# Kernel tuning notes

Hardware: AMD Instinct MI355X
Metric: run time of the kernel (lower is better)

The kernel has to match this reference:

```python
import jax, jax.numpy as jnp
import numpy as np

NV = 20000; NC = 20000; E = 500000
IN_SHAPE = 2; PE_DIM = 8; HID = 64; NL = 3
EPS = 1e-7  # GENConv message eps


def _lin(x, w, b):
    return x @ w + b


def _encode(x, pe, ew, eb, pw1, pb1, pw2, pb2):
    # relu(cat([Linear(x), 0.5*(pe_mlp(pe)+pe_mlp(-pe))], dim=1))
    def pe_mlp(p):
        return _lin(jax.nn.relu(_lin(p, pw1, pb1)), pw2, pb2)
    h = jnp.concatenate([_lin(x, ew, eb), 0.5 * (pe_mlp(pe) + pe_mlp(-pe))], axis=1)
    return jax.nn.relu(h)


def _genconv(x_src, x_dst, src, dst, ewt, lew, leb, w1, b1, w2, b2, n_dst):
    # GENConv(aggr='softmax', t=1, norm=None, msg_norm=False, edge_dim=1)
    msg = jax.nn.relu(x_src[src] + _lin(ewt, lew, leb)) + EPS  # [E, HID]
    m = jax.ops.segment_max(msg, dst, num_segments=n_dst)      # stable segment softmax
    ex = jnp.exp(msg - m[dst])
    s = jax.ops.segment_sum(ex, dst, num_segments=n_dst)
    agg = jax.ops.segment_sum(ex / (s[dst] + 1e-16) * msg, dst, num_segments=n_dst)
    out = agg + x_dst
    return _lin(jax.nn.relu(_lin(out, w1, b1)), w2, b2)  # MLP [hid -> 2hid -> hid]


def setup_inputs() -> dict:
    key = jax.random.key(0)
    ks = iter(jax.random.split(key, 64))
    d = {}
    d['x_vals'] = jax.random.normal(next(ks), (NV, IN_SHAPE), jnp.float32)
    d['x_cons'] = jax.random.normal(next(ks), (NC, IN_SHAPE), jnp.float32)
    d['pe_vals'] = jax.random.normal(next(ks), (NV, PE_DIM), jnp.float32)
    d['pe_cons'] = jax.random.normal(next(ks), (NC, PE_DIM), jnp.float32)
    d['edge_index_v2c'] = jnp.stack([
        jax.random.randint(next(ks), (E,), 0, NV),
        jax.random.randint(next(ks), (E,), 0, NC)])
    d['edge_index_c2v'] = jnp.stack([
        jax.random.randint(next(ks), (E,), 0, NC),
        jax.random.randint(next(ks), (E,), 0, NV)])
    d['edge_weight_v2c'] = jax.random.normal(next(ks), (E, 1), jnp.float32)
    d['edge_weight_c2v'] = jax.random.normal(next(ks), (E, 1), jnp.float32)
    def p(shape):
        return jax.random.normal(next(ks), shape, jnp.float32) * 0.05
    for k_ in ['vals', 'cons']:
        d[f'enc_{k_}_w'] = p((IN_SHAPE, HID // 2)); d[f'enc_{k_}_b'] = p((HID // 2,))
        d[f'pe_{k_}_w1'] = p((PE_DIM, HID)); d[f'pe_{k_}_b1'] = p((HID,))
        d[f'pe_{k_}_w2'] = p((HID, HID // 2)); d[f'pe_{k_}_b2'] = p((HID // 2,))
    for c in ['v2c', 'c2v']:
        d[f'{c}_edge_w'] = p((NL, 1, HID)); d[f'{c}_edge_b'] = p((NL, HID))
        d[f'{c}_w1'] = p((NL, HID, 2 * HID)); d[f'{c}_b1'] = p((NL, 2 * HID))
        d[f'{c}_w2'] = p((NL, 2 * HID, HID)); d[f'{c}_b2'] = p((NL, HID))
    for k_ in ['vals', 'cons']:
        d[f'pred_{k_}_w1'] = p((HID, HID)); d[f'pred_{k_}_b1'] = p((HID,))
        d[f'pred_{k_}_w2'] = p((HID, 1)); d[f'pred_{k_}_b2'] = p((1,))
    return d


def reference(x_vals, x_cons, pe_vals, pe_cons, edge_index_v2c, edge_index_c2v,
              edge_weight_v2c, edge_weight_c2v,
              enc_vals_w, enc_vals_b, pe_vals_w1, pe_vals_b1, pe_vals_w2, pe_vals_b2,
              enc_cons_w, enc_cons_b, pe_cons_w1, pe_cons_b1, pe_cons_w2, pe_cons_b2,
              v2c_edge_w, v2c_edge_b, v2c_w1, v2c_b1, v2c_w2, v2c_b2,
              c2v_edge_w, c2v_edge_b, c2v_w1, c2v_b1, c2v_w2, c2v_b2,
              pred_vals_w1, pred_vals_b1, pred_vals_w2, pred_vals_b2,
              pred_cons_w1, pred_cons_b1, pred_cons_w2, pred_cons_b2):
    vals = _encode(x_vals, pe_vals, enc_vals_w, enc_vals_b,
                   pe_vals_w1, pe_vals_b1, pe_vals_w2, pe_vals_b2)
    cons = _encode(x_cons, pe_cons, enc_cons_w, enc_cons_b,
                   pe_cons_w1, pe_cons_b1, pe_cons_w2, pe_cons_b2)
    hv, hc = [], []
    for i in range(NL):
        cons = _genconv(vals, cons, edge_index_v2c[0], edge_index_v2c[1],
                        edge_weight_v2c, v2c_edge_w[i], v2c_edge_b[i],
                        v2c_w1[i], v2c_b1[i], v2c_w2[i], v2c_b2[i], NC)
        vals = _genconv(cons, vals, edge_index_c2v[0], edge_index_c2v[1],
                        edge_weight_c2v, c2v_edge_w[i], c2v_edge_b[i],
                        c2v_w1[i], c2v_b1[i], c2v_w2[i], c2v_b2[i], NV)
        hc.append(cons); hv.append(vals)
    V = jnp.stack(hv)  # [NL, NV, HID]
    C = jnp.stack(hc)  # [NL, NC, HID]
    pv = _lin(jax.nn.relu(_lin(V, pred_vals_w1, pred_vals_b1)), pred_vals_w2, pred_vals_b2)
    pc = _lin(jax.nn.relu(_lin(C, pred_cons_w1, pred_cons_b1)), pred_cons_w2, pred_cons_b2)
    return pv[..., 0].T, pc[..., 0].T  # [NV, NL], [NC, NL]
```

## Files before the change

### kernel.cpp

```cpp
#include <hip/hip_runtime.h>

#define NVN 20000
#define NCN 20000
#define NE  500000
#define HID 64
#define NLAYER 3
#define TN 40
#define BSH 8
#define NB 79
#define P1E 2048

__device__ __forceinline__ float relu_(float x) { return fmaxf(x, 0.0f); }

__global__ __launch_bounds__(256) void binhist_kernel(
    const int* __restrict__ dstA, const int* __restrict__ dstB,
    int* __restrict__ binszA, int* __restrict__ binszB)
{
    __shared__ int cA[NB], cB[NB];
    int t = threadIdx.x;
    int e0 = blockIdx.x * P1E;
    if (t < NB) { cA[t] = 0; cB[t] = 0; }
    __syncthreads();
    for (int i = t; i < P1E; i += 256) {
        int e = e0 + i;
        if (e < NE) {
            atomicAdd(&cA[dstA[e] >> BSH], 1);
            atomicAdd(&cB[dstB[e] >> BSH], 1);
        }
    }
    __syncthreads();
    if (t < NB) {
        if (cA[t] > 0) atomicAdd(&binszA[t], cA[t]);
        if (cB[t] > 0) atomicAdd(&binszB[t], cB[t]);
    }
}

__global__ __launch_bounds__(256) void binscan_kernel(
    const int* __restrict__ binszA, int* __restrict__ binbaseA, int* __restrict__ bincurA,
    const int* __restrict__ binszB, int* __restrict__ binbaseB, int* __restrict__ bincurB)
{
    const int* binsz = blockIdx.x ? binszB : binszA;
    int* binbase     = blockIdx.x ? binbaseB : binbaseA;
    int* bincur      = blockIdx.x ? bincurB : bincurA;
    __shared__ int p[256];
    int t = threadIdx.x;
    p[t] = (t < NB) ? binsz[t] : 0;
    __syncthreads();
    for (int off = 1; off < 256; off <<= 1) {
        int v = (t >= off) ? p[t - off] : 0;
        __syncthreads();
        p[t] += v;
        __syncthreads();
    }
    if (t < NB) { int b = (t == 0) ? 0 : p[t - 1]; binbase[t] = b; bincur[t] = b; }
    if (t == NB) binbase[NB] = p[NB - 1];
}

__global__ __launch_bounds__(256) void scatter_p1_kernel(
    const int* __restrict__ eiA, const float* __restrict__ ewA,
    int* __restrict__ bincurA, int2* __restrict__ stageA,
    const int* __restrict__ eiB, const float* __restrict__ ewB,
    int* __restrict__ bincurB, int2* __restrict__ stageB)
{
    __shared__ int rnk[P1E];
    __shared__ int cnt[NB], base_[NB];
    int t = threadIdx.x;
    int e0 = blockIdx.x * P1E;

    for (int g = 0; g < 2; ++g) {
        const int* ei   = g ? eiB : eiA;
        const float* ew = g ? ewB : ewA;
        int* bincur     = g ? bincurB : bincurA;
        int2* stage     = g ? stageB : stageA;

        if (t < NB) cnt[t] = 0;
        __syncthreads();
        for (int i = t; i < P1E; i += 256) {
            int e = e0 + i;
            if (e < NE) {
                int d = ei[NE + e];
                rnk[i] = atomicAdd(&cnt[d >> BSH], 1);
            }
        }
        __syncthreads();
        if (t < NB && cnt[t] > 0) base_[t] = atomicAdd(&bincur[t], cnt[t]);
        __syncthreads();
        for (int i = t; i < P1E; i += 256) {
            int e = e0 + i;
            if (e < NE) {
                int s = ei[e], d = ei[NE + e];
                float w = ew[e];
                stage[base_[d >> BSH] + rnk[i]] =
                    make_int2((int)((unsigned)s | ((unsigned)d << 16)), __float_as_int(w));
            }
        }
        __syncthreads();
    }
}

__global__ __launch_bounds__(1024) void scatter_p2_kernel(
    const int* __restrict__ binbaseA, const int2* __restrict__ stageA,
    int* __restrict__ rowptrA, int2* __restrict__ pairA,
    const int* __restrict__ binbaseB, const int2* __restrict__ stageB,
    int* __restrict__ rowptrB, int2* __restrict__ pairB)
{
    __shared__ int deg[256], pfx[256], cur[256];
    int g = blockIdx.x / NB;
    int b = blockIdx.x % NB;
    const int* binbase = g ? binbaseB : binbaseA;
    const int2* stage  = g ? stageB : stageA;
    int* rowptr        = g ? rowptrB : rowptrA;
    int2* pair         = g ? pairB : pairA;

    int d0 = b << BSH;
    int d1 = min(d0 + 256, NCN);
    int nd = d1 - d0;
    int t = threadIdx.x;
    int estart = binbase[b], eend = binbase[b + 1];

    if (t < 256) deg[t] = 0;
    __syncthreads();
    for (int e = estart + t; e < eend; e += 1024) {
        int dst = (int)((unsigned)stage[e].x >> 16);
        atomicAdd(&deg[dst - d0], 1);
    }
    __syncthreads();
    if (t < 256) pfx[t] = deg[t];
    __syncthreads();
    for (int off = 1; off < 256; off <<= 1) {
        int v = (t >= off && t < 256) ? pfx[t - off] : 0;
        __syncthreads();
        if (t < 256) pfx[t] += v;
        __syncthreads();
    }
    if (t < nd) {
        int ex = estart + pfx[t] - deg[t];
        rowptr[d0 + t] = ex;
        cur[t] = ex;
    }
    if (t == 0) rowptr[d1] = eend;
    __syncthreads();
    for (int e = estart + t; e < eend; e += 1024) {
        int2 s = stage[e];
        unsigned u = (unsigned)s.x;
        int src = (int)(u & 0xFFFFu);
        int dst = (int)(u >> 16);
        int p = atomicAdd(&cur[dst - d0], 1);
        pair[p] = make_int2(src, s.y);
    }
}

__global__ __launch_bounds__(256) void encode2_kernel(
    const float* __restrict__ xv, const float* __restrict__ pev,
    const float* __restrict__ ewv, const float* __restrict__ ebv,
    const float* __restrict__ pw1v, const float* __restrict__ pb1v,
    const float* __restrict__ pw2v, const float* __restrict__ pb2v,
    const float* __restrict__ xc, const float* __restrict__ pec,
    const float* __restrict__ ewc, const float* __restrict__ ebc,
    const float* __restrict__ pw1c, const float* __restrict__ pb1c,
    const float* __restrict__ pw2c, const float* __restrict__ pb2c,
    float* __restrict__ outv, float* __restrict__ outc)
{
    __shared__ float sh[4][64];
    const int VB = (NVN + 3) / 4;
    int wave = threadIdx.x >> 6, lane = threadIdx.x & 63;
    int b = blockIdx.x;
    bool isC = (b >= VB);
    const float* x   = isC ? xc : xv;
    const float* pe  = isC ? pec : pev;
    const float* ew  = isC ? ewc : ewv;
    const float* eb  = isC ? ebc : ebv;
    const float* pw1 = isC ? pw1c : pw1v;
    const float* pb1 = isC ? pb1c : pb1v;
    const float* pw2 = isC ? pw2c : pw2v;
    const float* pb2 = isC ? pb2c : pb2v;
    float* out = isC ? outc : outv;
    int N = isC ? NCN : NVN;
    int n = (isC ? b - VB : b) * 4 + wave;
    if (n >= N) return;

    float accp = pb1[lane], accm = accp;
#pragma unroll
    for (int k = 0; k < 8; ++k) {
        float p = pe[n * 8 + k];
        float w = pw1[k * 64 + lane];
        accp += p * w;
        accm -= p * w;
    }
    float hs = 0.5f * (relu_(accp) + relu_(accm));
    float* my = sh[wave];
    my[lane] = hs;
    __builtin_amdgcn_wave_barrier();

    int col = lane & 31;
    float peo = pb2[col];
#pragma unroll
    for (int k = 0; k < 64; k += 4) {
        float4 hv = *(const float4*)(my + k);
        peo = fmaf(hv.x, pw2[(k + 0) * 32 + col], peo);
        peo = fmaf(hv.y, pw2[(k + 1) * 32 + col], peo);
        peo = fmaf(hv.z, pw2[(k + 2) * 32 + col], peo);
        peo = fmaf(hv.w, pw2[(k + 3) * 32 + col], peo);
    }
    float lino = x[n * 2 + 0] * ew[col] + x[n * 2 + 1] * ew[32 + col] + eb[col];
    float h = (lane < 32) ? lino : peo;
    out[n * 64 + lane] = relu_(h);
}

__global__ __launch_bounds__(256) void edge_agg_kernel(
    const float* __restrict__ xsrc,
    const float* __restrict__ xdst,
    const int* __restrict__ rowptr,
    const int2* __restrict__ pair,
    const float* __restrict__ lew,
    const float* __restrict__ leb,
    float* __restrict__ oa,
    int N)
{
    int wave = threadIdx.x >> 6, lane = threadIdx.x & 63;
    int n = blockIdx.x * 4 + wave;
    if (n >= N) return;

    int start = rowptr[n], end = rowptr[n + 1];
    float lw = lew[lane], lb = leb[lane];
    float xd = xdst[n * 64 + lane];

    float m0 = -1e30f, den0 = 0.0f, num0 = 0.0f;
    float m1 = -1e30f, den1 = 0.0f, num1 = 0.0f;
    int j = start;
    for (; j + 16 <= end; j += 16) {
        int idx[16]; float wv[16], msg[16];
#pragma unroll
        for (int c = 0; c < 16; ++c) {
            int2 p = pair[j + c];
            idx[c] = p.x;
            wv[c] = __int_as_float(p.y);
        }
#pragma unroll
        for (int c = 0; c < 16; ++c) {
            float xv = xsrc[idx[c] * 64 + lane];
            msg[c] = relu_(fmaf(wv[c], lw, xv + lb)) + 1e-7f;
        }
        {
            float a0 = fmaxf(msg[0], msg[1]), a1 = fmaxf(msg[2], msg[3]);
            float a2 = fmaxf(msg[4], msg[5]), a3 = fmaxf(msg[6], msg[7]);
            float mnew = fmaxf(m0, fmaxf(fmaxf(a0, a1), fmaxf(a2, a3)));
            float sc = __expf(m0 - mnew);
            float cd = 0.0f, cn = 0.0f;
#pragma unroll
            for (int c = 0; c < 8; ++c) {
                float e = __expf(msg[c] - mnew);
                cd += e;
                cn = fmaf(e, msg[c], cn);
            }
            den0 = fmaf(den0, sc, cd);
            num0 = fmaf(num0, sc, cn);
            m0 = mnew;
        }
        {
            float a0 = fmaxf(msg[8], msg[9]), a1 = fmaxf(msg[10], msg[11]);
            float a2 = fmaxf(msg[12], msg[13]), a3 = fmaxf(msg[14], msg[15]);
            float mnew = fmaxf(m1, fmaxf(fmaxf(a0, a1), fmaxf(a2, a3)));
            float sc = __expf(m1 - mnew);
            float cd = 0.0f, cn = 0.0f;
#pragma unroll
            for (int c = 8; c < 16; ++c) {
                float e = __expf(msg[c] - mnew);
                cd += e;
                cn = fmaf(e, msg[c], cn);
            }
            den1 = fmaf(den1, sc, cd);
            num1 = fmaf(num1, sc, cn);
            m1 = mnew;
        }
    }
    for (; j + 8 <= end; j += 8) {
        int idx[8]; float wv[8], msg[8];
#pragma unroll
        for (int c = 0; c < 8; ++c) {
            int2 p = pair[j + c];
            idx[c] = p.x;
            wv[c] = __int_as_float(p.y);
        }
#pragma unroll
        for (int c = 0; c < 8; ++c) {
            float xv = xsrc[idx[c] * 64 + lane];
            msg[c] = relu_(fmaf(wv[c], lw, xv + lb)) + 1e-7f;
        }
        float a0 = fmaxf(msg[0], msg[1]), a1 = fmaxf(msg[2], msg[3]);
        float a2 = fmaxf(msg[4], msg[5]), a3 = fmaxf(msg[6], msg[7]);
        float mnew = fmaxf(m0, fmaxf(fmaxf(a0, a1), fmaxf(a2, a3)));
        float sc = __expf(m0 - mnew);
        float cd = 0.0f, cn = 0.0f;
#pragma unroll
        for (int c = 0; c < 8; ++c) {
            float e = __expf(msg[c] - mnew);
            cd += e;
            cn = fmaf(e, msg[c], cn);
        }
        den0 = fmaf(den0, sc, cd);
        num0 = fmaf(num0, sc, cn);
        m0 = mnew;
    }
    for (; j < end; ++j) {
        int2 p = pair[j];
        float xv = xsrc[p.x * 64 + lane];
        float msg = relu_(fmaf(__int_as_float(p.y), lw, xv + lb)) + 1e-7f;
        float mnew = fmaxf(m0, msg);
        float sc = __expf(m0 - mnew);
        float e = __expf(msg - mnew);
        den0 = fmaf(den0, sc, e);
        num0 = fmaf(num0, sc, e * msg);
        m0 = mnew;
    }
    float M = fmaxf(m0, m1);
    float s0 = __expf(m0 - M), s1 = __expf(m1 - M);
    float den = den0 * s0 + den1 * s1;
    float num = num0 * s0 + num1 * s1;

    oa[n * 64 + lane] = num / (den + 1e-16f) + xd;
}

__global__ __launch_bounds__(256) void mlp_kernel(
    const float* __restrict__ oa,
    float* __restrict__ feat,
    const float* __restrict__ w1,
    const float* __restrict__ b1,
    const float* __restrict__ w2,
    const float* __restrict__ b2,
    const float* __restrict__ pw1,
    const float* __restrict__ pb1,
    const float* __restrict__ pw2,
    const float* __restrict__ pb2,
    float* __restrict__ outp,
    int N, int layer)
{
    __shared__ float w1s[64 * 128];
    __shared__ float w2s[128 * 64];
    __shared__ float pw1s[64 * 64];
    __shared__ float b1s[128];
    __shared__ float b2s[64];
    __shared__ float pb1s[64];
    __shared__ float pw2s[64];
    __shared__ float act[TN][68];
    __shared__ float hid[TN][132];

    int tid = threadIdx.x;
    for (int i = tid; i < 64 * 128; i += 256) w1s[i] = w1[i];
    for (int i = tid; i < 128 * 64; i += 256) w2s[i] = w2[i];
    for (int i = tid; i < 64 * 64; i += 256) pw1s[i] = pw1[i];
    if (tid < 128) b1s[tid] = b1[tid];
    if (tid < 64) { b2s[tid] = b2[tid]; pb1s[tid] = pb1[tid]; pw2s[tid] = pw2[tid]; }
    float pb2v = pb2[0];

    int o4 = (tid & 31) * 4;
    int o2 = (tid & 31) * 2;
    int n5 = (tid >> 5) * 5;
    __syncthreads();

    int ntiles = N / TN;
    for (int tile = blockIdx.x; tile < ntiles; tile += gridDim.x) {
        int base = tile * TN;
        {
            const float* g = oa + (size_t)base * 64;
            for (int i = tid; i < TN * 64; i += 256)
                act[i >> 6][i & 63] = g[i];
        }
        __syncthreads();

        {
            float acc[5][4];
#pragma unroll
            for (int i = 0; i < 5; ++i)
#pragma unroll
                for (int q = 0; q < 4; ++q) acc[i][q] = b1s[o4 + q];
            for (int k = 0; k < 64; k += 4) {
                float4 a[5];
#pragma unroll
                for (int i = 0; i < 5; ++i) a[i] = *(const float4*)&act[n5 + i][k];
                float4 w0 = *(const float4*)&w1s[(k + 0) * 128 + o4];
                float4 wq1 = *(const float4*)&w1s[(k + 1) * 128 + o4];
                float4 wq2 = *(const float4*)&w1s[(k + 2) * 128 + o4];
                float4 wq3 = *(const float4*)&w1s[(k + 3) * 128 + o4];
#pragma unroll
                for (int i = 0; i < 5; ++i) {
                    acc[i][0] = fmaf(a[i].x, w0.x, acc[i][0]);
                    acc[i][1] = fmaf(a[i].x, w0.y, acc[i][1]);
                    acc[i][2] = fmaf(a[i].x, w0.z, acc[i][2]);
                    acc[i][3] = fmaf(a[i].x, w0.w, acc[i][3]);
                    acc[i][0] = fmaf(a[i].y, wq1.x, acc[i][0]);
                    acc[i][1] = fmaf(a[i].y, wq1.y, acc[i][1]);
                    acc[i][2] = fmaf(a[i].y, wq1.z, acc[i][2]);
                    acc[i][3] = fmaf(a[i].y, wq1.w, acc[i][3]);
                    acc[i][0] = fmaf(a[i].z, wq2.x, acc[i][0]);
                    acc[i][1] = fmaf(a[i].z, wq2.y, acc[i][1]);
                    acc[i][2] = fmaf(a[i].z, wq2.z, acc[i][2]);
                    acc[i][3] = fmaf(a[i].z, wq2.w, acc[i][3]);
                    acc[i][0] = fmaf(a[i].w, wq3.x, acc[i][0]);
                    acc[i][1] = fmaf(a[i].w, wq3.y, acc[i][1]);
                    acc[i][2] = fmaf(a[i].w, wq3.z, acc[i][2]);
                    acc[i][3] = fmaf(a[i].w, wq3.w, acc[i][3]);
                }
            }
#pragma unroll
            for (int i = 0; i < 5; ++i) {
                float4 h4 = make_float4(relu_(acc[i][0]), relu_(acc[i][1]),
                                        relu_(acc[i][2]), relu_(acc[i][3]));
                *(float4*)&hid[n5 + i][o4] = h4;
            }
        }
        __syncthreads();

        {
            float acc[5][2];
#pragma unroll
            for (int i = 0; i < 5; ++i) { acc[i][0] = b2s[o2]; acc[i][1] = b2s[o2 + 1]; }
            for (int k = 0; k < 128; k += 4) {
                float4 a[5];
#pragma unroll
                for (int i = 0; i < 5; ++i) a[i] = *(const float4*)&hid[n5 + i][k];
                float2 w0 = *(const float2*)&w2s[(k + 0) * 64 + o2];
                float2 wq1 = *(const float2*)&w2s[(k + 1) * 64 + o2];
                float2 wq2 = *(const float2*)&w2s[(k + 2) * 64 + o2];
                float2 wq3 = *(const float2*)&w2s[(k + 3) * 64 + o2];
#pragma unroll
                for (int i = 0; i < 5; ++i) {
                    acc[i][0] = fmaf(a[i].x, w0.x, acc[i][0]);
                    acc[i][1] = fmaf(a[i].x, w0.y, acc[i][1]);
                    acc[i][0] = fmaf(a[i].y, wq1.x, acc[i][0]);
                    acc[i][1] = fmaf(a[i].y, wq1.y, acc[i][1]);
                    acc[i][0] = fmaf(a[i].z, wq2.x, acc[i][0]);
                    acc[i][1] = fmaf(a[i].z, wq2.y, acc[i][1]);
                    acc[i][0] = fmaf(a[i].w, wq3.x, acc[i][0]);
                    acc[i][1] = fmaf(a[i].w, wq3.y, acc[i][1]);
                }
            }
#pragma unroll
            for (int i = 0; i < 5; ++i) {
                float2 r2 = make_float2(acc[i][0], acc[i][1]);
                *(float2*)&feat[(size_t)(base + n5 + i) * 64 + o2] = r2;
                *(float2*)&act[n5 + i][o2] = r2;
            }
        }
        __syncthreads();

        {
            float acc[5][2];
#pragma unroll
            for (int i = 0; i < 5; ++i) { acc[i][0] = pb1s[o2]; acc[i][1] = pb1s[o2 + 1]; }
            for (int k = 0; k < 64; k += 4) {
                float4 a[5];
#pragma unroll
                for (int i = 0; i < 5; ++i) a[i] = *(const float4*)&act[n5 + i][k];
                float2 w0 = *(const float2*)&pw1s[(k + 0) * 64 + o2];
                float2 wq1 = *(const float2*)&pw1s[(k + 1) * 64 + o2];
                float2 wq2 = *(const float2*)&pw1s[(k + 2) * 64 + o2];
                float2 wq3 = *(const float2*)&pw1s[(k + 3) * 64 + o2];
#pragma unroll
                for (int i = 0; i < 5; ++i) {
                    acc[i][0] = fmaf(a[i].x, w0.x, acc[i][0]);
                    acc[i][1] = fmaf(a[i].x, w0.y, acc[i][1]);
                    acc[i][0] = fmaf(a[i].y, wq1.x, acc[i][0]);
                    acc[i][1] = fmaf(a[i].y, wq1.y, acc[i][1]);
                    acc[i][0] = fmaf(a[i].z, wq2.x, acc[i][0]);
                    acc[i][1] = fmaf(a[i].z, wq2.y, acc[i][1]);
                    acc[i][0] = fmaf(a[i].w, wq3.x, acc[i][0]);
                    acc[i][1] = fmaf(a[i].w, wq3.y, acc[i][1]);
                }
            }
            float pw2a = pw2s[o2], pw2b = pw2s[o2 + 1];
            float ps[5];
#pragma unroll
            for (int i = 0; i < 5; ++i)
                ps[i] = relu_(acc[i][0]) * pw2a + relu_(acc[i][1]) * pw2b;
#pragma unroll
            for (int msk = 16; msk >= 1; msk >>= 1) {
#pragma unroll
                for (int i = 0; i < 5; ++i)
                    ps[i] += __shfl_xor(ps[i], msk, 64);
            }
            if ((tid & 31) == 0) {
#pragma unroll
                for (int i = 0; i < 5; ++i)
                    outp[(size_t)(base + n5 + i) * NLAYER + layer] = ps[i] + pb2v;
            }
        }
        __syncthreads();
    }
}

extern "C" void kernel_launch(void* const* d_in, const int* in_sizes, int n_in,
                              void* d_out, int out_size, void* d_ws, size_t ws_size,
                              hipStream_t stream)
{
    const float* x_vals   = (const float*)d_in[0];
    const float* x_cons   = (const float*)d_in[1];
    const float* pe_vals  = (const float*)d_in[2];
    const float* pe_cons  = (const float*)d_in[3];
    const int*   ei_v2c   = (const int*)d_in[4];
    const int*   ei_c2v   = (const int*)d_in[5];
    const float* ew_v2c   = (const float*)d_in[6];
    const float* ew_c2v   = (const float*)d_in[7];
    const float* enc_vals_w = (const float*)d_in[8];
    const float* enc_vals_b = (const float*)d_in[9];
    const float* pe_vals_w1 = (const float*)d_in[10];
    const float* pe_vals_b1 = (const float*)d_in[11];
    const float* pe_vals_w2 = (const float*)d_in[12];
    const float* pe_vals_b2 = (const float*)d_in[13];
    const float* enc_cons_w = (const float*)d_in[14];
    const float* enc_cons_b = (const float*)d_in[15];
    const float* pe_cons_w1 = (const float*)d_in[16];
    const float* pe_cons_b1 = (const float*)d_in[17];
    const float* pe_cons_w2 = (const float*)d_in[18];
    const float* pe_cons_b2 = (const float*)d_in[19];
    const float* v2c_edge_w = (const float*)d_in[20];
    const float* v2c_edge_b = (const float*)d_in[21];
    const float* v2c_w1     = (const float*)d_in[22];
    const float* v2c_b1     = (const float*)d_in[23];
    const float* v2c_w2     = (const float*)d_in[24];
    const float* v2c_b2     = (const float*)d_in[25];
    const float* c2v_edge_w = (const float*)d_in[26];
    const float* c2v_edge_b = (const float*)d_in[27];
    const float* c2v_w1     = (const float*)d_in[28];
    const float* c2v_b1     = (const float*)d_in[29];
    const float* c2v_w2     = (const float*)d_in[30];
    const float* c2v_b2     = (const float*)d_in[31];
    const float* pred_vals_w1 = (const float*)d_in[32];
    const float* pred_vals_b1 = (const float*)d_in[33];
    const float* pred_vals_w2 = (const float*)d_in[34];
    const float* pred_vals_b2 = (const float*)d_in[35];
    const float* pred_cons_w1 = (const float*)d_in[36];
    const float* pred_cons_b1 = (const float*)d_in[37];
    const float* pred_cons_w2 = (const float*)d_in[38];
    const float* pred_cons_b2 = (const float*)d_in[39];

    float* out = (float*)d_out;
    float* out_c = out + (size_t)NVN * NLAYER;

    const size_t NF = (size_t)NVN * 64;

    float* ws     = (float*)d_ws;
    float* feat_v = ws;
    float* feat_c = feat_v + NF;
    float* oa     = feat_c + NF;
    int2* v2c_pair  = (int2*)(oa + NF);
    int2* c2v_pair  = v2c_pair + NE;
    int2* v2c_stage = c2v_pair + NE;
    int2* c2v_stage = v2c_stage + NE;
    int* ip = (int*)(c2v_stage + NE);
    int* v2c_binsz   = ip; ip += NB;
    int* c2v_binsz   = ip; ip += NB;
    int* v2c_binbase = ip; ip += NB + 1;
    int* c2v_binbase = ip; ip += NB + 1;
    int* v2c_bincur  = ip; ip += NB;
    int* c2v_bincur  = ip; ip += NB;
    int* v2c_rowptr  = ip; ip += NCN + 1;
    int* c2v_rowptr  = ip; ip += NVN + 1;

    const int p1b = (NE + P1E - 1) / P1E;

    hipMemsetAsync(v2c_binsz, 0, (size_t)(2 * NB) * sizeof(int), stream);
    binhist_kernel<<<p1b, 256, 0, stream>>>(ei_v2c + NE, ei_c2v + NE,
                                            v2c_binsz, c2v_binsz);
    binscan_kernel<<<2, 256, 0, stream>>>(v2c_binsz, v2c_binbase, v2c_bincur,
                                          c2v_binsz, c2v_binbase, c2v_bincur);
    scatter_p1_kernel<<<p1b, 256, 0, stream>>>(
        ei_v2c, ew_v2c, v2c_bincur, v2c_stage,
        ei_c2v, ew_c2v, c2v_bincur, c2v_stage);
    scatter_p2_kernel<<<2 * NB, 1024, 0, stream>>>(
        v2c_binbase, v2c_stage, v2c_rowptr, v2c_pair,
        c2v_binbase, c2v_stage, c2v_rowptr, c2v_pair);

    encode2_kernel<<<(NVN + 3) / 4 + (NCN + 3) / 4, 256, 0, stream>>>(
        x_vals, pe_vals, enc_vals_w, enc_vals_b,
        pe_vals_w1, pe_vals_b1, pe_vals_w2, pe_vals_b2,
        x_cons, pe_cons, enc_cons_w, enc_cons_b,
        pe_cons_w1, pe_cons_b1, pe_cons_w2, pe_cons_b2,
        feat_v, feat_c);

    for (int i = 0; i < NLAYER; ++i) {
        edge_agg_kernel<<<(NCN + 3) / 4, 256, 0, stream>>>(
            feat_v, feat_c, v2c_rowptr, v2c_pair,
            v2c_edge_w + (size_t)i * HID, v2c_edge_b + (size_t)i * HID,
            oa, NCN);
        mlp_kernel<<<250, 256, 0, stream>>>(
            oa, feat_c,
            v2c_w1 + (size_t)i * 8192, v2c_b1 + (size_t)i * 128,
            v2c_w2 + (size_t)i * 8192, v2c_b2 + (size_t)i * 64,
            pred_cons_w1, pred_cons_b1, pred_cons_w2, pred_cons_b2,
            out_c, NCN, i);
        edge_agg_kernel<<<(NVN + 3) / 4, 256, 0, stream>>>(
            feat_c, feat_v, c2v_rowptr, c2v_pair,
            c2v_edge_w + (size_t)i * HID, c2v_edge_b + (size_t)i * HID,
            oa, NVN);
        mlp_kernel<<<250, 256, 0, stream>>>(
            oa, feat_v,
            c2v_w1 + (size_t)i * 8192, c2v_b1 + (size_t)i * 128,
            c2v_w2 + (size_t)i * 8192, c2v_b2 + (size_t)i * 64,
            pred_vals_w1, pred_vals_b1, pred_vals_w2, pred_vals_b2,
            out, NVN, i);
    }
}
```

Measured before the change: 517.7 us.

## Replace bin histogram pass with fixed-capacity bin arenas; pad edge-agg tail

Drops the separate histogram and scan kernels (and a memset) by giving each destination bin a fixed-capacity staging arena of CAP entries and computing the bin offsets inside scatter_p2 from the final atomic cursors. This removes one full pass over the edge destinations and two launches. The risk is overflow if any bin gets more than CAP edges; with uniform random indices this is unlikely but not guaranteed. The edge aggregation tail now runs one masked 16-wide block instead of an 8-wide loop plus scalar leftovers, which cuts serial per-edge exp chains at the cost of redundant loads.

```diff
diff --git a/kernel.cpp b/kernel.cpp
--- a/kernel.cpp
+++ b/kernel.cpp
@@ -8,52 +8,16 @@
 #define TN 40
 #define BSH 8
 #define NB 79
+#define CAP 8192
 #define P1E 2048
 
 __device__ __forceinline__ float relu_(float x) { return fmaxf(x, 0.0f); }
 
-__global__ __launch_bounds__(256) void binhist_kernel(
-    const int* __restrict__ dstA, const int* __restrict__ dstB,
-    int* __restrict__ binszA, int* __restrict__ binszB)
-{
-    __shared__ int cA[NB], cB[NB];
+__global__ __launch_bounds__(256) void bininit_kernel(
+    int* __restrict__ bincurA, int* __restrict__ bincurB)
+{
     int t = threadIdx.x;
-    int e0 = blockIdx.x * P1E;
-    if (t < NB) { cA[t] = 0; cB[t] = 0; }
-    __syncthreads();
-    for (int i = t; i < P1E; i += 256) {
-        int e = e0 + i;
-        if (e < NE) {
-            atomicAdd(&cA[dstA[e] >> BSH], 1);
-            atomicAdd(&cB[dstB[e] >> BSH], 1);
-        }
-    }
-    __syncthreads();
-    if (t < NB) {
-        if (cA[t] > 0) atomicAdd(&binszA[t], cA[t]);
-        if (cB[t] > 0) atomicAdd(&binszB[t], cB[t]);
-    }
-}
-
-__global__ __launch_bounds__(256) void binscan_kernel(
-    const int* __restrict__ binszA, int* __restrict__ binbaseA, int* __restrict__ bincurA,
-    const int* __restrict__ binszB, int* __restrict__ binbaseB, int* __restrict__ bincurB)
-{
-    const int* binsz = blockIdx.x ? binszB : binszA;
-    int* binbase     = blockIdx.x ? binbaseB : binbaseA;
-    int* bincur      = blockIdx.x ? bincurB : bincurA;
-    __shared__ int p[256];
-    int t = threadIdx.x;
-    p[t] = (t < NB) ? binsz[t] : 0;
-    __syncthreads();
-    for (int off = 1; off < 256; off <<= 1) {
-        int v = (t >= off) ? p[t - off] : 0;
-        __syncthreads();
-        p[t] += v;
-        __syncthreads();
-    }
-    if (t < NB) { int b = (t == 0) ? 0 : p[t - 1]; binbase[t] = b; bincur[t] = b; }
-    if (t == NB) binbase[NB] = p[NB - 1];
+    if (t < NB) { bincurA[t] = t * CAP; bincurB[t] = t * CAP; }
 }
 
 __global__ __launch_bounds__(256) void scatter_p1_kernel(
@@ -99,28 +63,40 @@
 }
 
 __global__ __launch_bounds__(1024) void scatter_p2_kernel(
-    const int* __restrict__ binbaseA, const int2* __restrict__ stageA,
+    const int* __restrict__ bincurA, const int2* __restrict__ stageA,
     int* __restrict__ rowptrA, int2* __restrict__ pairA,
-    const int* __restrict__ binbaseB, const int2* __restrict__ stageB,
+    const int* __restrict__ bincurB, const int2* __restrict__ stageB,
     int* __restrict__ rowptrB, int2* __restrict__ pairB)
 {
+    __shared__ int p[128];
     __shared__ int deg[256], pfx[256], cur[256];
     int g = blockIdx.x / NB;
     int b = blockIdx.x % NB;
-    const int* binbase = g ? binbaseB : binbaseA;
-    const int2* stage  = g ? stageB : stageA;
-    int* rowptr        = g ? rowptrB : rowptrA;
-    int2* pair         = g ? pairB : pairA;
+    const int* bincur = g ? bincurB : bincurA;
+    const int2* stage = g ? stageB : stageA;
+    int* rowptr       = g ? rowptrB : rowptrA;
+    int2* pair        = g ? pairB : pairA;
+
+    int t = threadIdx.x;
+    if (t < 128) p[t] = (t < NB) ? (bincur[t] - t * CAP) : 0;
+    __syncthreads();
+    for (int off = 1; off < 128; off <<= 1) {
+        int v = (t >= off && t < 128) ? p[t - off] : 0;
+        __syncthreads();
+        if (t < 128) p[t] += v;
+        __syncthreads();
+    }
+    int base = (b == 0) ? 0 : p[b - 1];
+    int sz   = p[b] - base;
 
     int d0 = b << BSH;
     int d1 = min(d0 + 256, NCN);
     int nd = d1 - d0;
-    int t = threadIdx.x;
-    int estart = binbase[b], eend = binbase[b + 1];
+    int astart = b * CAP;
 
     if (t < 256) deg[t] = 0;
     __syncthreads();
-    for (int e = estart + t; e < eend; e += 1024) {
+    for (int e = astart + t; e < astart + sz; e += 1024) {
         int dst = (int)((unsigned)stage[e].x >> 16);
         atomicAdd(&deg[dst - d0], 1);
     }
@@ -134,19 +110,19 @@
         __syncthreads();
     }
     if (t < nd) {
-        int ex = estart + pfx[t] - deg[t];
+        int ex = base + pfx[t] - deg[t];
         rowptr[d0 + t] = ex;
         cur[t] = ex;
     }
-    if (t == 0) rowptr[d1] = eend;
+    if (t == 0) rowptr[d1] = base + sz;
     __syncthreads();
-    for (int e = estart + t; e < eend; e += 1024) {
+    for (int e = astart + t; e < astart + sz; e += 1024) {
         int2 s = stage[e];
         unsigned u = (unsigned)s.x;
         int src = (int)(u & 0xFFFFu);
         int dst = (int)(u >> 16);
-        int p = atomicAdd(&cur[dst - d0], 1);
-        pair[p] = make_int2(src, s.y);
+        int q = atomicAdd(&cur[dst - d0], 1);
+        pair[q] = make_int2(src, s.y);
     }
 }
 
@@ -274,44 +250,56 @@
             m1 = mnew;
         }
     }
-    for (; j + 8 <= end; j += 8) {
-        int idx[8]; float wv[8], msg[8];
-#pragma unroll
-        for (int c = 0; c < 8; ++c) {
-            int2 p = pair[j + c];
+    if (j < end) {
+        int last = end - 1;
+        int idx[16]; float wv[16], msg[16]; bool val[16];
+#pragma unroll
+        for (int c = 0; c < 16; ++c) {
+            int jj = j + c;
+            val[c] = jj < end;
+            int jc = val[c] ? jj : last;
+            int2 p = pair[jc];
             idx[c] = p.x;
             wv[c] = __int_as_float(p.y);
         }
 #pragma unroll
-        for (int c = 0; c < 8; ++c) {
+        for (int c = 0; c < 16; ++c) {
             float xv = xsrc[idx[c] * 64 + lane];
-            msg[c] = relu_(fmaf(wv[c], lw, xv + lb)) + 1e-7f;
-        }
-        float a0 = fmaxf(msg[0], msg[1]), a1 = fmaxf(msg[2], msg[3]);
-        float a2 = fmaxf(msg[4], msg[5]), a3 = fmaxf(msg[6], msg[7]);
-        float mnew = fmaxf(m0, fmaxf(fmaxf(a0, a1), fmaxf(a2, a3)));
-        float sc = __expf(m0 - mnew);
-        float cd = 0.0f, cn = 0.0f;
-#pragma unroll
-        for (int c = 0; c < 8; ++c) {
-            float e = __expf(msg[c] - mnew);
-            cd += e;
-            cn = fmaf(e, msg[c], cn);
-        }
-        den0 = fmaf(den0, sc, cd);
-        num0 = fmaf(num0, sc, cn);
-        m0 = mnew;
-    }
-    for (; j < end; ++j) {
-        int2 p = pair[j];
-        float xv = xsrc[p.x * 64 + lane];
-        float msg = relu_(fmaf(__int_as_float(p.y), lw, xv + lb)) + 1e-7f;
-        float mnew = fmaxf(m0, msg);
-        float sc = __expf(m0 - mnew);
-        float e = __expf(msg - mnew);
-        den0 = fmaf(den0, sc, e);
-        num0 = fmaf(num0, sc, e * msg);
-        m0 = mnew;
+            float tm = relu_(fmaf(wv[c], lw, xv + lb)) + 1e-7f;
+            msg[c] = val[c] ? tm : -1e30f;
+        }
+        {
+            float a0 = fmaxf(msg[0], msg[1]), a1 = fmaxf(msg[2], msg[3]);
+            float a2 = fmaxf(msg[4], msg[5]), a3 = fmaxf(msg[6], msg[7]);
+            float mnew = fmaxf(m0, fmaxf(fmaxf(a0, a1), fmaxf(a2, a3)));
+            float sc = __expf(m0 - mnew);
+            float cd = 0.0f, cn = 0.0f;
+#pragma unroll
+            for (int c = 0; c < 8; ++c) {
+                float e = __expf(msg[c] - mnew);
+                cd += e;
+                cn = fmaf(e, msg[c], cn);
+            }
+            den0 = fmaf(den0, sc, cd);
+            num0 = fmaf(num0, sc, cn);
+            m0 = mnew;
+        }
+        {
+            float a0 = fmaxf(msg[8], msg[9]), a1 = fmaxf(msg[10], msg[11]);
+            float a2 = fmaxf(msg[12], msg[13]), a3 = fmaxf(msg[14], msg[15]);
+            float mnew = fmaxf(m1, fmaxf(fmaxf(a0, a1), fmaxf(a2, a3)));
+            float sc = __expf(m1 - mnew);
+            float cd = 0.0f, cn = 0.0f;
+#pragma unroll
+            for (int c = 8; c < 16; ++c) {
+                float e = __expf(msg[c] - mnew);
+                cd += e;
+                cn = fmaf(e, msg[c], cn);
+            }
+            den1 = fmaf(den1, sc, cd);
+            num1 = fmaf(num1, sc, cn);
+            m1 = mnew;
+        }
     }
     float M = fmaxf(m0, m1);
     float s0 = __expf(m0 - M), s1 = __expf(m1 - M);
@@ -538,6 +526,7 @@
     float* out_c = out + (size_t)NVN * NLAYER;
 
     const size_t NF = (size_t)NVN * 64;
+    const size_t ARENA = (size_t)NB * CAP;
 
     float* ws     = (float*)d_ws;
     float* feat_v = ws;
@@ -546,12 +535,8 @@
     int2* v2c_pair  = (int2*)(oa + NF);
     int2* c2v_pair  = v2c_pair + NE;
     int2* v2c_stage = c2v_pair + NE;
-    int2* c2v_stage = v2c_stage + NE;
-    int* ip = (int*)(c2v_stage + NE);
-    int* v2c_binsz   = ip; ip += NB;
-    int* c2v_binsz   = ip; ip += NB;
-    int* v2c_binbase = ip; ip += NB + 1;
-    int* c2v_binbase = ip; ip += NB + 1;
+    int2* c2v_stage = v2c_stage + ARENA;
+    int* ip = (int*)(c2v_stage + ARENA);
     int* v2c_bincur  = ip; ip += NB;
     int* c2v_bincur  = ip; ip += NB;
     int* v2c_rowptr  = ip; ip += NCN + 1;
@@ -559,17 +544,13 @@
 
     const int p1b = (NE + P1E - 1) / P1E;
 
-    hipMemsetAsync(v2c_binsz, 0, (size_t)(2 * NB) * sizeof(int), stream);
-    binhist_kernel<<<p1b, 256, 0, stream>>>(ei_v2c + NE, ei_c2v + NE,
-                                            v2c_binsz, c2v_binsz);
-    binscan_kernel<<<2, 256, 0, stream>>>(v2c_binsz, v2c_binbase, v2c_bincur,
-                                          c2v_binsz, c2v_binbase, c2v_bincur);
+    bininit_kernel<<<1, 256, 0, stream>>>(v2c_bincur, c2v_bincur);
     scatter_p1_kernel<<<p1b, 256, 0, stream>>>(
         ei_v2c, ew_v2c, v2c_bincur, v2c_stage,
         ei_c2v, ew_c2v, c2v_bincur, c2v_stage);
     scatter_p2_kernel<<<2 * NB, 1024, 0, stream>>>(
-        v2c_binbase, v2c_stage, v2c_rowptr, v2c_pair,
-        c2v_binbase, c2v_stage, c2v_rowptr, c2v_pair);
+        v2c_bincur, v2c_stage, v2c_rowptr, v2c_pair,
+        c2v_bincur, c2v_stage, c2v_rowptr, c2v_pair);
 
     encode2_kernel<<<(NVN + 3) / 4 + (NCN + 3) / 4, 256, 0, stream>>>(
         x_vals, pe_vals, enc_vals_w, enc_vals_b,
```

After: 515.8 us. About the same (-0.4%).
